# Kernel tuning notes

Hardware: AMD Instinct MI355X
Metric: run time of the kernel (lower is better)

The kernel has to match this reference:

```python
import jax, jax.numpy as jnp
import numpy as np
import itertools

SKS = 3
GROUPS = 8
PAD = (SKS - 1) // 2


def setup_inputs() -> dict:
    key = jax.random.key(0)
    k1, k2 = jax.random.split(key)
    B, C, D, H, W = 2, 64, 64, 64, 64
    x = jax.random.normal(k1, (B, C, D, H, W), dtype=jnp.float32)
    w = jax.random.normal(k2, (B, GROUPS, SKS ** 3, D, H, W), dtype=jnp.float32)
    return {"x": x, "w": w}


def reference(x, w):
    # x: [B, C, D, H, W]; w: [B, G, sks^3, D, H, W]
    B, C, D, H, W = x.shape
    G = GROUPS
    # group the channels: [B, G, C//G, D, H, W]
    xg = x.reshape(B, G, C // G, D, H, W)
    offsets = list(itertools.product(range(-PAD, PAD + 1), repeat=3))  # (di, hi, wi), 27 taps
    out = jnp.zeros_like(xg)
    for k, (di, hi, wi) in enumerate(offsets):
        # circular shift matching torch.roll(x_g, (-di,-hi,-wi), dims=(2,3,4))
        shifted = jnp.roll(xg, shift=(-di, -hi, -wi), axis=(3, 4, 5))
        # broadcast per-group dynamic weight over the C//G channels in the group
        out = out + shifted * w[:, :, k][:, :, None]  # [B,G,C//G,D,H,W]
    return out.reshape(B, C, D, H, W)
```

## Files before the change

### kernel.cpp

```cpp
#include <hip/hip_runtime.h>


#define ND 64
#define NH 64
#define NW 64
#define HW 4096
#define DHW 262144

typedef const __attribute__((address_space(1))) unsigned int* gp_as1;
typedef __attribute__((address_space(3))) unsigned int* lp_as3;

__global__ __launch_bounds__(256, 2) void ska3d_kernel(const float* __restrict__ x,
                                                       const float* __restrict__ w,
                                                       float* __restrict__ out) {
    __shared__ float lds[4][8][6][NW];

    const int tid  = threadIdx.x;
    const int lane = tid & 63;
    const int wv   = tid >> 6;
    const int w0   = (lane & 15) * 4;
    const int hl   = lane >> 4;
    const int c0   = wv * 2;

    const int bid = blockIdx.x;
    const int dc  = bid & 7;
    const int ht  = (bid >> 3) & 15;
    const int g   = (bid >> 7) & 7;
    const int b   = bid >> 10;

    const int d0 = dc * 8;
    const int h0 = ht * 4;
    const int h  = h0 + hl;

    const float* xb = x + (size_t)(b * 64 + g * 8) * DHW;
    const float* wb = w + (size_t)(b * 8 + g) * 27 * DHW + h * NW + w0;
    float* ob = out + (size_t)(b * 64 + g * 8 + c0) * DHW + h * NW + w0;

    const int wl = (w0 + 63) & 63;
    const int wr = (w0 + 4) & 63;

#define STAGE(p) do {                                                          \
        const int slot_ = (p) & 3;                                             \
        const int dd_   = (p) & 63;                                            \
        _Pragma("unroll")                                                      \
        for (int i = 0; i < 3; ++i) {                                          \
            const int fid = i * 256 + tid;                         \
            const int c_  = fid / 96;                                          \
            const int rm_ = fid - c_ * 96;                                     \
            const int r_  = rm_ >> 4;                                \
            const int ws_ = rm_ & 15;                               \
            const int hh_ = (h0 - 1 + r_) & 63;                                \
            const float* gsrc = xb + (size_t)c_ * DHW + dd_ * HW + hh_ * NW + ws_ * 4; \
            __builtin_amdgcn_global_load_lds((gp_as1)gsrc,                     \
                (lp_as3)&lds[slot_][c_][r_][ws_ * 4], 16, 0, 0);               \
        }                                                                      \
    } while (0)

#define LOADW(dp) do {                                                         \
        const float* wpn_ = wb + (size_t)(dp) * HW;                            \
        _Pragma("unroll")                                                      \
        for (int k = 0; k < 27; ++k)                                           \
            wk[k] = *(const float4*)(wpn_ + (size_t)k * DHW);                  \
    } while (0)

    float4 wk[27];

    STAGE(d0 - 1);
    STAGE(d0);
    STAGE(d0 + 1);
    LOADW(d0);
    asm volatile("s_waitcnt vmcnt(0)" ::: "memory");

#pragma unroll 1
    for (int i = 0; i < 8; ++i) {
        const int d = d0 + i;

        asm volatile("s_waitcnt vmcnt(29)" ::: "memory");
        asm volatile("s_barrier" ::: "memory");

        if (i < 7) STAGE(d + 2);

        float acc[2][4];
#pragma unroll
        for (int cc = 0; cc < 2; ++cc)
            acc[cc][0] = acc[cc][1] = acc[cc][2] = acc[cc][3] = 0.f;

#pragma unroll
        for (int di = -1; di <= 1; ++di) {
            const int slot = (d + di) & 3;
#pragma unroll
            for (int hi = -1; hi <= 1; ++hi) {
                const int r  = hl + hi + 1;
                const int kb = (di + 1) * 9 + (hi + 1) * 3;
#pragma unroll
                for (int cc = 0; cc < 2; ++cc) {
                    const float* row = &lds[slot][c0 + cc][r][0];
                    const float  xm = row[wl];
                    const float4 xv = *(const float4*)(row + w0);
                    const float  xp = row[wr];
                    const float4 wa = wk[kb], wm = wk[kb + 1], wc = wk[kb + 2];
                    acc[cc][0] += wa.x * xm;    acc[cc][1] += wa.y * xv.x;
                    acc[cc][2] += wa.z * xv.y;  acc[cc][3] += wa.w * xv.z;
                    acc[cc][0] += wm.x * xv.x;  acc[cc][1] += wm.y * xv.y;
                    acc[cc][2] += wm.z * xv.z;  acc[cc][3] += wm.w * xv.w;
                    acc[cc][0] += wc.x * xv.y;  acc[cc][1] += wc.y * xv.z;
                    acc[cc][2] += wc.z * xv.w;  acc[cc][3] += wc.w * xp;
                }
            }
        }

#pragma unroll
        for (int cc = 0; cc < 2; ++cc)
            *(float4*)(ob + (size_t)cc * DHW + (size_t)d * HW) =
                make_float4(acc[cc][0], acc[cc][1], acc[cc][2], acc[cc][3]);

        if (i < 7) LOADW(d + 1);
    }
}

extern "C" void kernel_launch(void* const* d_in, const int* in_sizes, int n_in,
                              void* d_out, int out_size, void* d_ws, size_t ws_size,
                              hipStream_t stream) {
    const float* x = (const float*)d_in[0];
    const float* w = (const float*)d_in[1];
    float* out = (float*)d_out;
    dim3 grid(2048);
    dim3 block(256);
    hipLaunchKernelGGL(ska3d_kernel, grid, block, 0, stream, x, w, out);
}
```

Before: 170.0 us.

## Enlarge H tile to 8 rows with padded LDS rows and block swizzle

Blocks grow to 512 threads covering 8 H rows instead of 4, which cuts the redundant H-halo staging of x. LDS rows are padded to 72 floats with the circular W-wrap neighbours staged explicitly, so the inner loop indexes without modulo. The change also adds a block-index swizzle that reorders block-to-tile assignment and nontemporal output stores. The cost is an uneven staging loop where some threads issue fewer loads, and heavier per-block register and LDS use.

```diff
diff --git a/kernel.cpp b/kernel.cpp
--- a/kernel.cpp
+++ b/kernel.cpp
@@ -6,61 +6,68 @@
 #define NW 64
 #define HW 4096
 #define DHW 262144
+#define ROWF 72
 
 typedef const __attribute__((address_space(1))) unsigned int* gp_as1;
 typedef __attribute__((address_space(3))) unsigned int* lp_as3;
+typedef float f32x4 __attribute__((ext_vector_type(4)));
 
-__global__ __launch_bounds__(256, 2) void ska3d_kernel(const float* __restrict__ x,
-                                                       const float* __restrict__ w,
-                                                       float* __restrict__ out) {
-    __shared__ float lds[4][8][6][NW];
+__global__ __launch_bounds__(512)
+__attribute__((amdgpu_waves_per_eu(1, 2)))
+void ska3d_kernel(const float* __restrict__ x,
+                  const float* __restrict__ w,
+                  float* __restrict__ out) {
+    __shared__ float lds[4][8][10][ROWF];
 
     const int tid  = threadIdx.x;
     const int lane = tid & 63;
     const int wv   = tid >> 6;
-    const int w0   = (lane & 15) * 4;
+    const int j    = lane & 15;
+    const int w0   = j * 4;
     const int hl   = lane >> 4;
-    const int c0   = wv * 2;
+    const int c0   = wv & 6;
+    const int rh   = (wv & 1) * 4;
 
-    const int bid = blockIdx.x;
-    const int dc  = bid & 7;
-    const int ht  = (bid >> 3) & 15;
-    const int g   = (bid >> 7) & 7;
-    const int b   = bid >> 10;
+    const int bid  = blockIdx.x;
+    const int sbid = (bid & 7) * 128 + (bid >> 3);
+    const int dc   = sbid & 7;
+    const int ht   = (sbid >> 3) & 7;
+    const int g    = (sbid >> 6) & 7;
+    const int b    = sbid >> 9;
 
     const int d0 = dc * 8;
-    const int h0 = ht * 4;
-    const int h  = h0 + hl;
+    const int h0 = ht * 8;
+    const int h  = h0 + rh + hl;
 
     const float* xb = x + (size_t)(b * 64 + g * 8) * DHW;
     const float* wb = w + (size_t)(b * 8 + g) * 27 * DHW + h * NW + w0;
     float* ob = out + (size_t)(b * 64 + g * 8 + c0) * DHW + h * NW + w0;
 
-    const int wl = (w0 + 63) & 63;
-    const int wr = (w0 + 4) & 63;
-
 #define STAGE(p) do {                                                          \
         const int slot_ = (p) & 3;                                             \
         const int dd_   = (p) & 63;                                            \
         _Pragma("unroll")                                                      \
-        for (int i = 0; i < 3; ++i) {                                          \
-            const int fid = i * 256 + tid;                         \
-            const int c_  = fid / 96;                                          \
-            const int rm_ = fid - c_ * 96;                                     \
-            const int r_  = rm_ >> 4;                                \
-            const int ws_ = rm_ & 15;                               \
-            const int hh_ = (h0 - 1 + r_) & 63;                                \
-            const float* gsrc = xb + (size_t)c_ * DHW + dd_ * HW + hh_ * NW + ws_ * 4; \
-            __builtin_amdgcn_global_load_lds((gp_as1)gsrc,                     \
-                (lp_as3)&lds[slot_][c_][r_][ws_ * 4], 16, 0, 0);               \
+        for (int i_ = 0; i_ < 3; ++i_) {                                       \
+            const int fid = i_ * 512 + tid;                       \
+            if (fid < 1440) {                                                  \
+                const int c_  = fid / 180;                                     \
+                const int rm_ = fid - c_ * 180;                                \
+                const int r_  = rm_ / 18;                            \
+                const int u_  = rm_ - r_ * 18;                      \
+                const int hh_ = (h0 - 1 + r_) & 63;                            \
+                const int sw_ = (u_ == 0) ? 60 : ((u_ == 17) ? 0 : (u_ - 1) * 4); \
+                const float* gsrc = xb + (size_t)c_ * DHW + dd_ * HW + hh_ * NW + sw_; \
+                __builtin_amdgcn_global_load_lds((gp_as1)gsrc,                 \
+                    (lp_as3)&lds[slot_][c_][r_][u_ * 4], 16, 0, 0);            \
+            }                                                                  \
         }                                                                      \
     } while (0)
 
 #define LOADW(dp) do {                                                         \
-        const float* wpn_ = wb + (size_t)(dp) * HW;                            \
+        const float* wp_ = wb + (size_t)(dp) * HW;                             \
         _Pragma("unroll")                                                      \
-        for (int k = 0; k < 27; ++k)                                           \
-            wk[k] = *(const float4*)(wpn_ + (size_t)k * DHW);                  \
+        for (int k_ = 0; k_ < 27; ++k_)                                        \
+            wk[k_] = *(const float4*)(wp_ + (size_t)k_ * DHW);                 \
     } while (0)
 
     float4 wk[27];
@@ -90,14 +97,14 @@
             const int slot = (d + di) & 3;
 #pragma unroll
             for (int hi = -1; hi <= 1; ++hi) {
-                const int r  = hl + hi + 1;
+                const int r  = rh + hl + hi + 1;
                 const int kb = (di + 1) * 9 + (hi + 1) * 3;
 #pragma unroll
                 for (int cc = 0; cc < 2; ++cc) {
                     const float* row = &lds[slot][c0 + cc][r][0];
-                    const float  xm = row[wl];
-                    const float4 xv = *(const float4*)(row + w0);
-                    const float  xp = row[wr];
+                    const float  xm = row[3 + w0];
+                    const float4 xv = *(const float4*)(row + 4 + w0);
+                    const float  xp = row[8 + w0];
                     const float4 wa = wk[kb], wm = wk[kb + 1], wc = wk[kb + 2];
                     acc[cc][0] += wa.x * xm;    acc[cc][1] += wa.y * xv.x;
                     acc[cc][2] += wa.z * xv.y;  acc[cc][3] += wa.w * xv.z;
@@ -110,9 +117,12 @@
         }
 
 #pragma unroll
-        for (int cc = 0; cc < 2; ++cc)
-            *(float4*)(ob + (size_t)cc * DHW + (size_t)d * HW) =
-                make_float4(acc[cc][0], acc[cc][1], acc[cc][2], acc[cc][3]);
+        for (int cc = 0; cc < 2; ++cc) {
+            f32x4 v;
+            v.x = acc[cc][0]; v.y = acc[cc][1]; v.z = acc[cc][2]; v.w = acc[cc][3];
+            __builtin_nontemporal_store(v,
+                (f32x4*)(ob + (size_t)cc * DHW + (size_t)d * HW));
+        }
 
         if (i < 7) LOADW(d + 1);
     }
@@ -124,7 +134,7 @@
     const float* x = (const float*)d_in[0];
     const float* w = (const float*)d_in[1];
     float* out = (float*)d_out;
-    dim3 grid(2048);
-    dim3 block(256);
+    dim3 grid(1024);
+    dim3 block(512);
     hipLaunchKernelGGL(ska3d_kernel, grid, block, 0, stream, x, w, out);
 }
```

Result: slower. 219.3 us (+29.0%).
